# Optimization experiments

Hardware: AMD Instinct MI355X
Metric: run time of the kernel (lower is better)

## Reference

```python
import jax, jax.numpy as jnp
import numpy as np

EPS = 1e-5


def setup_inputs() -> dict:
    key = jax.random.key(0)
    k_x, k_y, k_w, k_b = jax.random.split(key, 4)
    B, IN, OUT = 16384, 1024, 1024
    x = jax.random.normal(k_x, (B, IN), dtype=jnp.float32)
    y = jax.random.normal(k_y, (B, OUT), dtype=jnp.float32)
    # nn.Linear default init scale ~ 1/sqrt(in_features); keep activations sane
    weight = jax.random.normal(k_w, (OUT, IN), dtype=jnp.float32) / np.sqrt(IN)
    bias = jax.random.normal(k_b, (OUT,), dtype=jnp.float32) / np.sqrt(IN)
    gamma = jnp.ones((OUT,), dtype=jnp.float32)
    beta = jnp.zeros((OUT,), dtype=jnp.float32)
    return {"x": x, "y": y, "weight": weight, "bias": bias, "gamma": gamma, "beta": beta}


def reference(x, y, weight, bias, gamma, beta):
    # Linear: z[b, o] = sum_i x[b, i] * weight[o, i] + bias[o]
    z = jnp.einsum('bi,oi->bo', x, weight) + bias
    # LayerNorm over the feature (out_features) dim, biased variance
    mean = jnp.mean(z, axis=-1, keepdims=True)
    var = jnp.mean(jnp.square(z), axis=-1, keepdims=True) - jnp.square(mean)
    ln = (z - mean) * jax.lax.rsqrt(var + EPS) * gamma + beta
    # residual add then elementwise multiply
    return (ln + y) * y
```

## Files before the change

### kernel.cpp

```cpp
#include <hip/hip_runtime.h>
#include <stdint.h>

typedef unsigned short u16;
typedef __attribute__((ext_vector_type(8))) short short8;
typedef __attribute__((ext_vector_type(4))) float floatx4;
typedef __attribute__((ext_vector_type(2))) float floatx2;

#define K_DIM 1024
#define N_DIM 1024
#define BM 64
#define BK 32
#define NCHUNK (K_DIM / BK)

__device__ __forceinline__ u16 f2b(float f) {
    union { float f; uint32_t i; } v; v.f = f;
    uint32_t u = v.i;
    return (u16)((u + 0x7FFFu + ((u >> 16) & 1u)) >> 16);
}
__device__ __forceinline__ float b2f(u16 u) {
    union { uint32_t i; float f; } v; v.i = ((uint32_t)u) << 16; return v.f;
}

__global__ __launch_bounds__(256) void convert_w_kernel(const float* __restrict__ w,
                                                        u16* __restrict__ wbf) {
    int idx = (blockIdx.x * 256 + threadIdx.x) * 8;
    floatx4 a = *(const floatx4*)(w + idx);
    floatx4 b = *(const floatx4*)(w + idx + 4);
    short8 o;
    o[0] = (short)f2b(a[0]); o[1] = (short)f2b(a[1]);
    o[2] = (short)f2b(a[2]); o[3] = (short)f2b(a[3]);
    o[4] = (short)f2b(b[0]); o[5] = (short)f2b(b[1]);
    o[6] = (short)f2b(b[2]); o[7] = (short)f2b(b[3]);
    *(short8*)(wbf + idx) = o;
}

__global__ __launch_bounds__(1024) void fused_gemm_ln_kernel(
    const float* __restrict__ x, const float* __restrict__ y,
    const u16* __restrict__ wbf, const float* __restrict__ bias,
    const float* __restrict__ gamma, const float* __restrict__ beta,
    float* __restrict__ out)
{
    __shared__ __align__(16) u16 lds_a[2][BM * BK];
    __shared__ __align__(16) u16 zbuf[16 * 1024];
    __shared__ float ls_sum[64];
    __shared__ float ls_sum2[64];
    __shared__ float ls_mean[64];
    __shared__ float ls_rs[64];

    const int tid  = threadIdx.x;
    const int lane = tid & 63;
    const int wv   = tid >> 6;
    const int q    = lane >> 4;
    const int row0 = blockIdx.x * BM;

    if (tid < 64) { ls_sum[tid] = 0.0f; ls_sum2[tid] = 0.0f; }

    const int sr = tid >> 4;
    const int sk = (tid & 15) << 1;
    const float* s_src = x + (size_t)(row0 + sr) * K_DIM + sk;
    const int s_qs  = (sk >> 3) ^ ((sr >> 1) & 3);
    const int s_off = sr * 64 + s_qs * 16 + (sk & 7) * 2;

    const u16* wrow = wbf + (size_t)((wv << 6) + (lane & 15)) * K_DIM + (q << 3);

    int a_off[4];
#pragma unroll
    for (int mi = 0; mi < 4; ++mi) {
        int r  = (mi << 4) + (lane & 15);
        int qs = q ^ ((r >> 1) & 3);
        a_off[mi] = r * (BK * 2) + qs * 16;
    }

    floatx4 acc[4][4];
#pragma unroll
    for (int mi = 0; mi < 4; ++mi)
#pragma unroll
        for (int ni = 0; ni < 4; ++ni)
            acc[mi][ni] = (floatx4){0.0f, 0.0f, 0.0f, 0.0f};

    {
        floatx2 v = *(const floatx2*)(s_src);
        uint32_t p = (uint32_t)f2b(v[0]) | ((uint32_t)f2b(v[1]) << 16);
        *(uint32_t*)((char*)(&lds_a[0][0]) + s_off) = p;
    }

    for (int kc = 0; kc < NCHUNK; ++kc) {
        const int cur = kc & 1;
        const bool pf = (kc + 1 < NCHUNK);
        floatx2 vn;
        if (pf) vn = *(const floatx2*)(s_src + (kc + 1) * BK);

        __syncthreads();

        short8 bfrag[4];
        const u16* wp = wrow + kc * BK;
#pragma unroll
        for (int ni = 0; ni < 4; ++ni)
            bfrag[ni] = *(const short8*)(wp + ni * (16 * K_DIM));

        short8 afrag[4];
        const char* abase = (const char*)(&lds_a[cur][0]);
#pragma unroll
        for (int mi = 0; mi < 4; ++mi)
            afrag[mi] = *(const short8*)(abase + a_off[mi]);

#pragma unroll
        for (int mi = 0; mi < 4; ++mi)
#pragma unroll
            for (int ni = 0; ni < 4; ++ni)
                acc[mi][ni] = __builtin_amdgcn_mfma_f32_16x16x32_bf16(
                    afrag[mi], bfrag[ni], acc[mi][ni], 0, 0, 0);

        if (pf) {
            uint32_t p = (uint32_t)f2b(vn[0]) | ((uint32_t)f2b(vn[1]) << 16);
            *(uint32_t*)((char*)(&lds_a[cur ^ 1][0]) + s_off) = p;
        }
    }

    float bias_v[4];
#pragma unroll
    for (int ni = 0; ni < 4; ++ni)
        bias_v[ni] = bias[(wv << 6) + (ni << 4) + (lane & 15)];
#pragma unroll
    for (int mi = 0; mi < 4; ++mi)
#pragma unroll
        for (int ni = 0; ni < 4; ++ni)
#pragma unroll
            for (int r = 0; r < 4; ++r)
                acc[mi][ni][r] += bias_v[ni];

#pragma unroll
    for (int mi = 0; mi < 4; ++mi)
#pragma unroll
        for (int r = 0; r < 4; ++r) {
            float s = 0.0f, s2 = 0.0f;
#pragma unroll
            for (int ni = 0; ni < 4; ++ni) {
                float v = acc[mi][ni][r];
                s += v; s2 += v * v;
            }
#pragma unroll
            for (int m = 1; m < 16; m <<= 1) {
                s  += __shfl_xor(s,  m, 64);
                s2 += __shfl_xor(s2, m, 64);
            }
            if ((lane & 15) == 0) {
                int rl = (mi << 4) + (q << 2) + r;
                atomicAdd(&ls_sum[rl], s);
                atomicAdd(&ls_sum2[rl], s2);
            }
        }

    __syncthreads();
    if (tid < 64) {
        float mean = ls_sum[tid] * (1.0f / 1024.0f);
        float var  = ls_sum2[tid] * (1.0f / 1024.0f) - mean * mean;
        ls_mean[tid] = mean;
        ls_rs[tid]   = rsqrtf(var + 1e-5f);
    }

    for (int mi = 0; mi < 4; ++mi) {
#pragma unroll
        for (int ni = 0; ni < 4; ++ni)
#pragma unroll
            for (int r = 0; r < 4; ++r) {
                int lr   = (q << 2) + r;
                int lin  = (((wv << 6) + (ni << 4) + (lane & 15)) << 1);
                int phys = lr * 2048 + (lin ^ (q << 5));
                *(u16*)((char*)zbuf + phys) = f2b(acc[mi][ni][r]);
            }
        __syncthreads();
#pragma unroll
        for (int it = 0; it < 2; ++it) {
            int row  = (tid >> 7) + (it << 3);
            int c8   = tid & 127;
            int phys = row * 2048 + ((c8 << 4) ^ (((row >> 2) & 3) << 5));
            short8 z8 = *(const short8*)((const char*)zbuf + phys);
            int grow  = row0 + (mi << 4) + row;
            float mean = ls_mean[(mi << 4) + row];
            float rs   = ls_rs[(mi << 4) + row];
            const float* yp = y     + (size_t)grow * N_DIM + c8 * 8;
            const float* gp = gamma + c8 * 8;
            const float* bp = beta  + c8 * 8;
            float*       op = out   + (size_t)grow * N_DIM + c8 * 8;
            floatx4 y0 = *(const floatx4*)(yp);
            floatx4 y1 = *(const floatx4*)(yp + 4);
            floatx4 g0 = *(const floatx4*)(gp);
            floatx4 g1 = *(const floatx4*)(gp + 4);
            floatx4 b0 = *(const floatx4*)(bp);
            floatx4 b1 = *(const floatx4*)(bp + 4);
            floatx4 o0, o1;
#pragma unroll
            for (int e = 0; e < 4; ++e) {
                float zv = b2f((u16)z8[e]);
                o0[e] = ((zv - mean) * rs * g0[e] + b0[e] + y0[e]) * y0[e];
            }
#pragma unroll
            for (int e = 0; e < 4; ++e) {
                float zv = b2f((u16)z8[e + 4]);
                o1[e] = ((zv - mean) * rs * g1[e] + b1[e] + y1[e]) * y1[e];
            }
            *(floatx4*)(op)     = o0;
            *(floatx4*)(op + 4) = o1;
        }
        __syncthreads();
    }
}

extern "C" void kernel_launch(void* const* d_in, const int* in_sizes, int n_in,
                              void* d_out, int out_size, void* d_ws, size_t ws_size,
                              hipStream_t stream) {
    const float* x     = (const float*)d_in[0];
    const float* y     = (const float*)d_in[1];
    const float* wgt   = (const float*)d_in[2];
    const float* bias  = (const float*)d_in[3];
    const float* gamma = (const float*)d_in[4];
    const float* beta  = (const float*)d_in[5];
    float* out = (float*)d_out;
    u16* wbf = (u16*)d_ws;

    const int wElems = in_sizes[2];
    convert_w_kernel<<<wElems / (256 * 8), 256, 0, stream>>>(wgt, wbf);

    const int M = in_sizes[0] / K_DIM;
    fused_gemm_ln_kernel<<<M / BM, 1024, 0, stream>>>(x, y, wbf, bias, gamma, beta, out);
}
```

Baseline: 252.4 us.

## Pre-pack weights into MFMA fragment order and double-buffer B fragments in registers

The weight conversion kernel now writes bf16 weights in a tiled layout that matches the MFMA B-fragment order, so each lane's 16-byte load per chunk is contiguous across the wave instead of strided by K rows. The main loop also prefetches the next chunk's B fragments into a second register buffer ahead of the MFMAs, with the loop unrolled by 2. This targets uncoalesced global weight loads and the load latency exposed in the K loop, at the cost of extra VGPRs in a 1024-thread block.

After: 229.1 us. 1.1x faster.

```diff
diff --git a/kernel.cpp b/kernel.cpp
--- a/kernel.cpp
+++ b/kernel.cpp
@@ -21,22 +21,28 @@
     union { uint32_t i; float f; } v; v.i = ((uint32_t)u) << 16; return v.f;
 }
 
-__global__ __launch_bounds__(256) void convert_w_kernel(const float* __restrict__ w,
-                                                        u16* __restrict__ wbf) {
-    int idx = (blockIdx.x * 256 + threadIdx.x) * 8;
-    floatx4 a = *(const floatx4*)(w + idx);
-    floatx4 b = *(const floatx4*)(w + idx + 4);
+__global__ __launch_bounds__(256) void pack_w_kernel(const float* __restrict__ w,
+                                                     u16* __restrict__ wpk) {
+    int gid  = blockIdx.x * 256 + threadIdx.x;
+    int lane = gid & 63;
+    int kc   = (gid >> 6) & 31;
+    int tile = gid >> 11;
+    int n = tile * 16 + (lane & 15);
+    int k = kc * 32 + (lane >> 4) * 8;
+    const float* src = w + (size_t)n * K_DIM + k;
+    floatx4 a = *(const floatx4*)(src);
+    floatx4 b = *(const floatx4*)(src + 4);
     short8 o;
     o[0] = (short)f2b(a[0]); o[1] = (short)f2b(a[1]);
     o[2] = (short)f2b(a[2]); o[3] = (short)f2b(a[3]);
     o[4] = (short)f2b(b[0]); o[5] = (short)f2b(b[1]);
     o[6] = (short)f2b(b[2]); o[7] = (short)f2b(b[3]);
-    *(short8*)(wbf + idx) = o;
+    *(short8*)(wpk + (size_t)gid * 8) = o;
 }
 
 __global__ __launch_bounds__(1024) void fused_gemm_ln_kernel(
     const float* __restrict__ x, const float* __restrict__ y,
-    const u16* __restrict__ wbf, const float* __restrict__ bias,
+    const u16* __restrict__ wpk, const float* __restrict__ bias,
     const float* __restrict__ gamma, const float* __restrict__ beta,
     float* __restrict__ out)
 {
@@ -61,15 +67,9 @@
     const int s_qs  = (sk >> 3) ^ ((sr >> 1) & 3);
     const int s_off = sr * 64 + s_qs * 16 + (sk & 7) * 2;
 
-    const u16* wrow = wbf + (size_t)((wv << 6) + (lane & 15)) * K_DIM + (q << 3);
-
-    int a_off[4];
-#pragma unroll
-    for (int mi = 0; mi < 4; ++mi) {
-        int r  = (mi << 4) + (lane & 15);
-        int qs = q ^ ((r >> 1) & 3);
-        a_off[mi] = r * (BK * 2) + qs * 16;
-    }
+    const u16* bp = wpk + (size_t)wv * 65536 + lane * 8;
+
+    const int a_base = (lane & 15) * 64 + (q ^ (((lane & 15) >> 1) & 3)) * 16;
 
     floatx4 acc[4][4];
 #pragma unroll
@@ -83,33 +83,38 @@
         uint32_t p = (uint32_t)f2b(v[0]) | ((uint32_t)f2b(v[1]) << 16);
         *(uint32_t*)((char*)(&lds_a[0][0]) + s_off) = p;
     }
-
+    short8 bfr[2][4];
+#pragma unroll
+    for (int ni = 0; ni < 4; ++ni)
+        bfr[0][ni] = *(const short8*)(bp + ni * 16384);
+
+#pragma unroll 2
     for (int kc = 0; kc < NCHUNK; ++kc) {
         const int cur = kc & 1;
         const bool pf = (kc + 1 < NCHUNK);
+
+        __syncthreads();
+
+        short8 afrag[4];
+        const char* ab = (const char*)(&lds_a[cur][0]);
+#pragma unroll
+        for (int mi = 0; mi < 4; ++mi)
+            afrag[mi] = *(const short8*)(ab + a_base + mi * 1024);
+
         floatx2 vn;
-        if (pf) vn = *(const floatx2*)(s_src + (kc + 1) * BK);
-
-        __syncthreads();
-
-        short8 bfrag[4];
-        const u16* wp = wrow + kc * BK;
-#pragma unroll
-        for (int ni = 0; ni < 4; ++ni)
-            bfrag[ni] = *(const short8*)(wp + ni * (16 * K_DIM));
-
-        short8 afrag[4];
-        const char* abase = (const char*)(&lds_a[cur][0]);
-#pragma unroll
-        for (int mi = 0; mi < 4; ++mi)
-            afrag[mi] = *(const short8*)(abase + a_off[mi]);
+        if (pf) {
+#pragma unroll
+            for (int ni = 0; ni < 4; ++ni)
+                bfr[cur ^ 1][ni] = *(const short8*)(bp + ni * 16384 + (kc + 1) * 512);
+            vn = *(const floatx2*)(s_src + (kc + 1) * BK);
+        }
 
 #pragma unroll
         for (int mi = 0; mi < 4; ++mi)
 #pragma unroll
             for (int ni = 0; ni < 4; ++ni)
                 acc[mi][ni] = __builtin_amdgcn_mfma_f32_16x16x32_bf16(
-                    afrag[mi], bfrag[ni], acc[mi][ni], 0, 0, 0);
+                    afrag[mi], bfr[cur][ni], acc[mi][ni], 0, 0, 0);
 
         if (pf) {
             uint32_t p = (uint32_t)f2b(vn[0]) | ((uint32_t)f2b(vn[1]) << 16);
@@ -181,14 +186,14 @@
             float rs   = ls_rs[(mi << 4) + row];
             const float* yp = y     + (size_t)grow * N_DIM + c8 * 8;
             const float* gp = gamma + c8 * 8;
-            const float* bp = beta  + c8 * 8;
+            const float* bpv = beta + c8 * 8;
             float*       op = out   + (size_t)grow * N_DIM + c8 * 8;
             floatx4 y0 = *(const floatx4*)(yp);
             floatx4 y1 = *(const floatx4*)(yp + 4);
             floatx4 g0 = *(const floatx4*)(gp);
             floatx4 g1 = *(const floatx4*)(gp + 4);
-            floatx4 b0 = *(const floatx4*)(bp);
-            floatx4 b1 = *(const floatx4*)(bp + 4);
+            floatx4 b0 = *(const floatx4*)(bpv);
+            floatx4 b1 = *(const floatx4*)(bpv + 4);
             floatx4 o0, o1;
 #pragma unroll
             for (int e = 0; e < 4; ++e) {
@@ -217,11 +222,10 @@
     const float* gamma = (const float*)d_in[4];
     const float* beta  = (const float*)d_in[5];
     float* out = (float*)d_out;
-    u16* wbf = (u16*)d_ws;
-
-    const int wElems = in_sizes[2];
-    convert_w_kernel<<<wElems / (256 * 8), 256, 0, stream>>>(wgt, wbf);
+    u16* wpk = (u16*)d_ws;
+
+    pack_w_kernel<<<512, 256, 0, stream>>>(wgt, wpk);
 
     const int M = in_sizes[0] / K_DIM;
-    fused_gemm_ln_kernel<<<M / BM, 1024, 0, stream>>>(x, y, wbf, bias, gamma, beta, out);
-}
+    fused_gemm_ln_kernel<<<M / BM, 1024, 0, stream>>>(x, y, wpk, bias, gamma, beta, out);
+}
```
